# Kernel optimization log

Measured on AMD Instinct MI355X. Metric: run time of the kernel, lower is better.

## Reference

```python
import jax, jax.numpy as jnp
import numpy as np

B, M = 1024, 200000
D_IN, DIM, D_OUT = 256, 128, 10
T = 1.0
EPS = 1e-7


def setup_inputs() -> dict:
    key = jax.random.key(0)
    k1, k2, k3, k4, k5 = jax.random.split(key, 5)
    x = jax.random.normal(k1, (B, D_IN), dtype=jnp.float32)
    y = jax.random.randint(k2, (B,), 0, D_OUT)
    candidate_x = jax.random.normal(k3, (M, D_IN), dtype=jnp.float32)
    candidate_y = jax.random.randint(k4, (M,), 0, D_OUT)
    W_enc = jax.random.normal(k5, (DIM, D_IN), dtype=jnp.float32) * (1.0 / np.sqrt(D_IN))
    b_enc = jnp.zeros((DIM,), dtype=jnp.float32)
    return {"x": x, "y": y, "candidate_x": candidate_x, "candidate_y": candidate_y,
            "W_enc": W_enc, "b_enc": b_enc, "is_train": 0}


def reference(x, y, candidate_x, candidate_y, W_enc, b_enc, is_train):
    # eval path (is_train == 0): no candidate subsampling, no diagonal masking
    h = x @ W_enc.T + b_enc            # [B, DIM]
    hc = candidate_x @ W_enc.T + b_enc  # [M, DIM]
    # pairwise L2 distance (cdist, p=2)
    sq = jnp.sum(h * h, axis=-1, keepdims=True) + jnp.sum(hc * hc, axis=-1)[None, :] \
         - 2.0 * (h @ hc.T)            # [B, M]
    dist = jnp.sqrt(jnp.maximum(sq, 0.0)) / T
    p = jax.nn.softmax(-dist, axis=-1)  # [B, M]
    y1h = jax.nn.one_hot(candidate_y, D_OUT, dtype=h.dtype)  # [M, D_OUT]
    logits = p @ y1h                    # [B, D_OUT]
    return jnp.log(logits + EPS)
```

## Files before the change

kernel.cpp:

```cpp
#include <hip/hip_runtime.h>
#include <hip/hip_bf16.h>
#include <math.h>

#define B_N   1024
#define M_N   200000
#define DIN   256
#define DIMN  128
#define DOUT  10
#define EPS_F 1e-7f
#define M_PAD 200064
#define NBY   1563
#define CTILES 8
#define NGRP  ((NBY + CTILES - 1)/CTILES)
#define YPAD  200

typedef __bf16 bf16_t;
typedef __bf16 bf16x8 __attribute__((ext_vector_type(8)));
typedef float  f32x4  __attribute__((ext_vector_type(4)));


__global__ void cvt_w_kernel(const float* __restrict__ W, bf16_t* __restrict__ Wb){
    int i = blockIdx.x*256 + threadIdx.x;
    if (i < DIMN*DIN) Wb[i] = (bf16_t)W[i];
}

__global__ void hist_kernel(const int* __restrict__ cy, int* __restrict__ hist){
    __shared__ int h[DOUT];
    if (threadIdx.x < DOUT) h[threadIdx.x] = 0;
    __syncthreads();
    for (int i = blockIdx.x*blockDim.x + threadIdx.x; i < M_N; i += gridDim.x*blockDim.x)
        atomicAdd(&h[cy[i]], 1);
    __syncthreads();
    if (threadIdx.x < DOUT) atomicAdd(&hist[threadIdx.x*16], h[threadIdx.x]);
}

__global__ void prefix_kernel(const int* __restrict__ hist, int* __restrict__ cs){
    if (threadIdx.x == 0 && blockIdx.x == 0){
        int acc = 0;
        for (int c = 0; c < DOUT; ++c){ cs[c] = acc; acc += hist[c*16]; }
        cs[DOUT] = acc;
    }
}


__global__ __launch_bounds__(256) void encode_kernel(
    const float* __restrict__ src, const bf16_t* __restrict__ Wb,
    bf16_t* __restrict__ out, float* __restrict__ onorm, int N,
    const int* __restrict__ ycls, int* __restrict__ counters,
    const int* __restrict__ cs)
{
    __shared__ bf16_t As[128][136];
    __shared__ int   posL[128];
    __shared__ float nbuf[128][2];
    __shared__ int   cntL[DOUT], baseL[DOUT];
    const int tid = threadIdx.x;
    const int r0  = blockIdx.x*128;

    int myc = -1, myrank = 0;
    if (ycls != nullptr){
        if (tid < DOUT) cntL[tid] = 0;
        __syncthreads();
        if (tid < 128 && r0 + tid < N){
            myc = ycls[r0 + tid];
            myrank = atomicAdd(&cntL[myc], 1);
        }
        __syncthreads();
        if (tid < DOUT && cntL[tid] > 0)
            baseL[tid] = atomicAdd(&counters[tid*16], cntL[tid]);
        __syncthreads();
    }
    if (tid < 128)
        posL[tid] = (myc >= 0) ? (cs[myc] + baseL[myc] + myrank) : (r0 + tid);

    const int lane = tid & 63, wid = tid >> 6;
    const int wr = wid >> 1, wc = wid & 1;
    const int l15 = lane & 15, quad = lane >> 4;
    const int cbase = wc*64;

    bf16x8 ball[2][4];
    #pragma unroll
    for (int kh = 0; kh < 2; ++kh)
        #pragma unroll
        for (int ks = 0; ks < 4; ++ks){
            ball[kh][ks] = *(const bf16x8*)(Wb + (size_t)(cbase + 0*16 + l15)*DIN + kh*128 + ks*32 + quad*8);
        }

    f32x4 acc[4][4] = {};
    #pragma unroll
    for (int kh = 0; kh < 2; ++kh){
        __syncthreads();
        #pragma unroll
        for (int i = 0; i < 8; ++i){
            int idx = i*256 + tid;
            int row = idx >> 4;
            int col = (idx & 15)*8;
            int rr  = r0 + row; if (rr > N-1) rr = N-1;
            const float4* p4 = (const float4*)(src + (size_t)rr*DIN + kh*128 + col);
            float4 f0 = p4[0], f1 = p4[1];
            bf16x8 v;
            v[0]=(bf16_t)f0.x; v[1]=(bf16_t)f0.y; v[2]=(bf16_t)f0.z; v[3]=(bf16_t)f0.w;
            v[4]=(bf16_t)f1.x; v[5]=(bf16_t)f1.y; v[6]=(bf16_t)f1.z; v[7]=(bf16_t)f1.w;
            *(bf16x8*)&As[row][col] = v;
        }
        __syncthreads();
        #pragma unroll
        for (int ks = 0; ks < 4; ++ks){
            const int k  = ks*32 + quad*8;
            const int kg = kh*128 + k;
            bf16x8 a[4], b[4];
            b[0] = ball[kh][ks];
            #pragma unroll
            for (int ct = 1; ct < 4; ++ct)
                b[ct] = *(const bf16x8*)(Wb + (size_t)(cbase + ct*16 + l15)*DIN + kg);
            #pragma unroll
            for (int rt = 0; rt < 4; ++rt)
                a[rt] = *(const bf16x8*)&As[wr*64 + rt*16 + l15][k];
            #pragma unroll
            for (int rt = 0; rt < 4; ++rt)
                #pragma unroll
                for (int ct = 0; ct < 4; ++ct)
                    acc[rt][ct] = __builtin_amdgcn_mfma_f32_16x16x32_bf16(a[rt], b[ct], acc[rt][ct], 0, 0, 0);
        }
    }

    float np[4][4];
    #pragma unroll
    for (int rt = 0; rt < 4; ++rt)
        #pragma unroll
        for (int r = 0; r < 4; ++r){
            float s = 0.f;
            #pragma unroll
            for (int ct = 0; ct < 4; ++ct){ float v = acc[rt][ct][r]; s += v*v; }
            np[rt][r] = s;
        }
    #pragma unroll
    for (int m = 1; m < 16; m <<= 1)
        #pragma unroll
        for (int rt = 0; rt < 4; ++rt)
            #pragma unroll
            for (int r = 0; r < 4; ++r)
                np[rt][r] += __shfl_xor(np[rt][r], m, 64);
    if (l15 == 0){
        #pragma unroll
        for (int rt = 0; rt < 4; ++rt)
            #pragma unroll
            for (int r = 0; r < 4; ++r)
                nbuf[wr*64 + rt*16 + quad*4 + r][wc] = np[rt][r];
    }

    __syncthreads();

    #pragma unroll
    for (int rt = 0; rt < 4; ++rt)
        #pragma unroll
        for (int r = 0; r < 4; ++r){
            int rl = wr*64 + rt*16 + quad*4 + r;
            #pragma unroll
            for (int ct = 0; ct < 4; ++ct)
                As[rl][cbase + ct*16 + l15] = (bf16_t)acc[rt][ct][r];
        }
    __syncthreads();

    {
        const int rsub = tid >> 4;
        const int cpos = (tid & 15)*8;
        #pragma unroll
        for (int p = 0; p < 8; ++p){
            int rl = p*16 + rsub;
            size_t rowp = (size_t)posL[rl]*DIMN;
            *(bf16x8*)(out + rowp + cpos) = *(const bf16x8*)&As[rl][cpos];
        }
    }
    if (tid < 128){
        int rs = r0 + tid;
        if (rs < N) onorm[posL[tid]] = nbuf[tid][0] + nbuf[tid][1];
    }
}


__device__ __forceinline__ void gld_lds16(const bf16_t* g, bf16_t* l){
    __builtin_amdgcn_global_load_lds((const __attribute__((address_space(1))) void*)g,
                                     (__attribute__((address_space(3))) void*)l, 16, 0, 0);
}

__device__ __forceinline__ void bfly16(float (&s)[2][4]){
    #pragma unroll
    for (int m = 1; m < 16; m <<= 1)
        #pragma unroll
        for (int rt = 0; rt < 2; ++rt)
            #pragma unroll
            for (int r = 0; r < 4; ++r)
                s[rt][r] += __shfl_xor(s[rt][r], m, 64);
}

__device__ __forceinline__ void flushC(float (&s)[2][4], int c, int rbase,
                                       int quad, int l15, float* __restrict__ accG){
    bfly16(s);
    if (l15 == 0){
        #pragma unroll
        for (int rt = 0; rt < 2; ++rt)
            #pragma unroll
            for (int r = 0; r < 4; ++r)
                atomicAdd(&accG[(size_t)(rbase + rt*16 + quad*4 + r)*16 + c], s[rt][r]);
    }
}

__global__ __launch_bounds__(512, 4) void fused_kernel(
    const bf16_t* __restrict__ hb, const bf16_t* __restrict__ hcb,
    const float* __restrict__ hn, const float* __restrict__ hcn,
    const int* __restrict__ csg, float* __restrict__ accG)
{
    const int lin = blockIdx.y*8 + blockIdx.x;
    const int i8  = lin & 7;
    const int t   = lin >> 3;
    const int q   = t >> 3;
    const int r8  = t & 7;
    const int bx  = r8;
    const int yg  = q*8 + i8;
    if (yg >= NGRP) return;

    __shared__ bf16_t Bs0[128][128];
    __shared__ bf16_t Bs1[128][128];
    const int tid = threadIdx.x;
    const int lane = tid & 63, wid = tid >> 6;
    const int wr = wid >> 1, wc = wid & 1;
    const int l15 = lane & 15, quad = lane >> 4;
    const int rbase = bx*128 + wr*32;

    bf16x8 a[4][2];
    #pragma unroll
    for (int ks = 0; ks < 4; ++ks)
        #pragma unroll
        for (int rt = 0; rt < 2; ++rt)
            a[ks][rt] = *(const bf16x8*)(hb + (size_t)(rbase + rt*16 + l15)*DIMN + ks*32 + quad*8);

    float hnv[2][4];
    #pragma unroll
    for (int rt = 0; rt < 2; ++rt)
        #pragma unroll
        for (int r = 0; r < 4; ++r)
            hnv[rt][r] = hn[rbase + rt*16 + quad*4 + r];

    int cseg[DOUT+1];
    #pragma unroll
    for (int i = 0; i <= DOUT; ++i) cseg[i] = __builtin_amdgcn_readfirstlane(csg[i]);

    const int by0 = yg*CTILES;
    int nt = NBY - by0; if (nt > CTILES) nt = CTILES;

    float s[2][4] = {};
    int curC = -1;

    auto stage = [&](bf16_t (&Bsb)[128][128], int by){
        const int cb = by*128;
        #pragma unroll
        for (int i = 0; i < 4; ++i){
            int c   = i*512 + tid;
            int col = c >> 4, j = c & 15;
            int cc  = cb + col; if (cc > M_N-1) cc = M_N-1;
            const bf16_t* g = hcb + (size_t)cc*DIMN + ((j ^ (col & 7)) << 3);
            bf16_t* l = &Bsb[0][0] + ((i*512 + (wid << 6)) << 3);
            gld_lds16(g, l);
        }
    };

    auto compute = [&](const bf16_t (&Bsb)[128][128], int by){
        const int cbase0 = by*128;
        f32x4 acc[2][4] = {};
        const char* bsb = (const char*)&Bsb[0][0];
        #pragma unroll
        for (int ks = 0; ks < 4; ++ks){
            bf16x8 b[4];
            #pragma unroll
            for (int ct = 0; ct < 4; ++ct){
                int row = wc*64 + ct*16 + l15;
                int off = (row << 8) + ((((ks << 6) + (quad << 4))) ^ ((l15 & 7) << 4));
                b[ct] = *(const bf16x8*)(bsb + off);
            }
            #pragma unroll
            for (int rt = 0; rt < 2; ++rt)
                #pragma unroll
                for (int ct = 0; ct < 4; ++ct)
                    acc[rt][ct] = __builtin_amdgcn_mfma_f32_16x16x32_bf16(a[ks][rt], b[ct], acc[rt][ct], 0, 0, 0);
        }

        float hcnv[4];
        #pragma unroll
        for (int ct = 0; ct < 4; ++ct){
            int cc = cbase0 + wc*64 + ct*16 + l15;
            hcnv[ct] = (cc < M_N) ? hcn[cc] : 1e30f;
        }
        #pragma unroll
        for (int rt = 0; rt < 2; ++rt)
            #pragma unroll
            for (int ct = 0; ct < 4; ++ct)
                #pragma unroll
                for (int r = 0; r < 4; ++r){
                    float sq = fmaxf(fmaf(-2.0f, acc[rt][ct][r], hnv[rt][r] + hcnv[ct]), 0.0f);
                    acc[rt][ct][r] = __expf(-__builtin_amdgcn_sqrtf(sq));
                }

        const int lastc = min(cbase0 + 127, M_N - 1);
        int cLo = 0, cHi = 0;
        #pragma unroll
        for (int c = 1; c < DOUT; ++c){
            if (cbase0 >= cseg[c]) cLo = c;
            if (lastc  >= cseg[c]) cHi = c;
        }

        if (cLo == curC && cHi == curC){
            #pragma unroll
            for (int rt = 0; rt < 2; ++rt)
                #pragma unroll
                for (int r = 0; r < 4; ++r){
                    float v0 = acc[rt][0][r] + acc[rt][1][r];
                    float v1 = acc[rt][2][r] + acc[rt][3][r];
                    s[rt][r] += v0 + v1;
                }
        } else {
            if (curC >= 0) flushC(s, curC, rbase, quad, l15, accG);
            #pragma unroll
            for (int rt = 0; rt < 2; ++rt)
                #pragma unroll
                for (int r = 0; r < 4; ++r) s[rt][r] = 0.f;
            for (int c = cLo; c <= cHi; ++c){
                const int s0 = cseg[c], s1 = cseg[c+1];
                float m[2][4];
                #pragma unroll
                for (int rt = 0; rt < 2; ++rt)
                    #pragma unroll
                    for (int r = 0; r < 4; ++r){
                        float v = 0.f;
                        #pragma unroll
                        for (int ct = 0; ct < 4; ++ct){
                            int cc = cbase0 + wc*64 + ct*16 + l15;
                            v += (cc >= s0 && cc < s1) ? acc[rt][ct][r] : 0.f;
                        }
                        m[rt][r] = v;
                    }
                if (c == cHi){
                    #pragma unroll
                    for (int rt = 0; rt < 2; ++rt)
                        #pragma unroll
                        for (int r = 0; r < 4; ++r) s[rt][r] = m[rt][r];
                    curC = cHi;
                } else {
                    flushC(m, c, rbase, quad, l15, accG);
                }
            }
        }
    };

    stage(Bs0, by0);
    __syncthreads();

    #pragma unroll 1
    for (int tp = 0; tp < CTILES/2; ++tp){
        int t0 = tp*2;
        if (t0 >= nt) break;
        if (t0 + 1 < nt) stage(Bs1, by0 + t0 + 1);
        compute(Bs0, by0 + t0);
        __syncthreads();
        int t1 = t0 + 1;
        if (t1 >= nt) break;
        if (t1 + 1 < nt) stage(Bs0, by0 + t1 + 1);
        compute(Bs1, by0 + t1);
        __syncthreads();
    }
    if (curC >= 0) flushC(s, curC, rbase, quad, l15, accG);
}

__global__ void finalize_kernel(const float* __restrict__ accG, float* __restrict__ out){
    int b = blockIdx.x*blockDim.x + threadIdx.x;
    if (b < B_N){
        float v[DOUT]; float den = 0.f;
        #pragma unroll
        for (int c = 0; c < DOUT; ++c){ v[c] = accG[b*16 + c]; den += v[c]; }
        float inv = (den > 0.f) ? 1.0f/den : 0.f;
        #pragma unroll
        for (int c = 0; c < DOUT; ++c) out[b*DOUT + c] = logf(v[c]*inv + EPS_F);
    }
}


extern "C" void kernel_launch(void* const* d_in, const int* in_sizes, int n_in,
                              void* d_out, int out_size, void* d_ws, size_t ws_size,
                              hipStream_t stream)
{
    const float* x  = (const float*)d_in[0];
    const float* cx = (const float*)d_in[2];
    const int*   cy = (const int*)d_in[3];
    const float* W  = (const float*)d_in[4];
    float* out = (float*)d_out;

    char* w = (char*)d_ws;
    size_t off = 0;
    bf16_t* hcb = (bf16_t*)(w + off); off += (size_t)M_PAD*DIMN*2;
    bf16_t* hb  = (bf16_t*)(w + off); off += (size_t)B_N*DIMN*2;
    float*  hcn = (float*) (w + off); off += (size_t)M_PAD*4;
    float*  hn  = (float*) (w + off); off += (size_t)B_N*4;
    bf16_t* Wb  = (bf16_t*)(w + off); off += (size_t)DIMN*DIN*2;
    size_t zoff = off;
    float* accG = (float*)(w + off); off += (size_t)B_N*16*4;
    int* hist     = (int*)(w + off); off += 16*DOUT*4;
    int* counters = (int*)(w + off); off += 16*DOUT*4;
    int* csg      = (int*)(w + off); off += 64;
    size_t zsize = off - zoff;

    hipMemsetAsync(w + zoff, 0, zsize, stream);
    cvt_w_kernel<<<dim3((DIMN*DIN + 255)/256), dim3(256), 0, stream>>>(W, Wb);
    hist_kernel<<<dim3(256), dim3(256), 0, stream>>>(cy, hist);
    prefix_kernel<<<dim3(1), dim3(1), 0, stream>>>(hist, csg);
    encode_kernel<<<dim3(M_PAD/128), dim3(256), 0, stream>>>(cx, Wb, hcb, hcn, M_N, cy, counters, csg);
    encode_kernel<<<dim3(B_N/128), dim3(256), 0, stream>>>(x, Wb, hb, hn, B_N, nullptr, nullptr, nullptr);
    fused_kernel<<<dim3(8, YPAD), dim3(512), 0, stream>>>(hb, hcb, hn, hcn, csg, accG);
    finalize_kernel<<<dim3((B_N + 255)/256), dim3(256), 0, stream>>>(accG, out);
}
```

Before: 482.4 us.

## Software-pipeline MFMA and epilogue across tiles, fold exp2 scaling, merge encode launches

```diff
diff --git a/kernel.cpp b/kernel.cpp
--- a/kernel.cpp
+++ b/kernel.cpp
@@ -9,14 +9,26 @@
 #define DOUT  10
 #define EPS_F 1e-7f
 #define M_PAD 200064
+#define MBLK  1563
 #define NBY   1563
 #define CTILES 8
 #define NGRP  ((NBY + CTILES - 1)/CTILES)
 #define YPAD  200
+#define L2E2  2.0813689810056077f
 
 typedef __bf16 bf16_t;
 typedef __bf16 bf16x8 __attribute__((ext_vector_type(8)));
 typedef float  f32x4  __attribute__((ext_vector_type(4)));
+
+__device__ __forceinline__ float fast_exp2(float x){
+#if __has_builtin(__builtin_amdgcn_exp2f)
+    return __builtin_amdgcn_exp2f(x);
+#else
+    float r;
+    asm("v_exp_f32 %0, %1" : "=v"(r) : "v"(x));
+    return r;
+#endif
+}
 
 
 __global__ void cvt_w_kernel(const float* __restrict__ W, bf16_t* __restrict__ Wb){
@@ -44,9 +56,11 @@
 
 
 __global__ __launch_bounds__(256) void encode_kernel(
-    const float* __restrict__ src, const bf16_t* __restrict__ Wb,
-    bf16_t* __restrict__ out, float* __restrict__ onorm, int N,
-    const int* __restrict__ ycls, int* __restrict__ counters,
+    const float* __restrict__ cx, const float* __restrict__ xb,
+    const bf16_t* __restrict__ Wb,
+    bf16_t* __restrict__ hcb, float* __restrict__ hcn,
+    bf16_t* __restrict__ hb,  float* __restrict__ hn,
+    const int* __restrict__ cy, int* __restrict__ counters,
     const int* __restrict__ cs)
 {
     __shared__ bf16_t As[128][136];
@@ -54,7 +68,13 @@
     __shared__ float nbuf[128][2];
     __shared__ int   cntL[DOUT], baseL[DOUT];
     const int tid = threadIdx.x;
-    const int r0  = blockIdx.x*128;
+
+    const float* src; bf16_t* out; float* onorm; int N; const int* ycls; int r0;
+    if ((int)blockIdx.x < MBLK){
+        src = cx; out = hcb; onorm = hcn; N = M_N; ycls = cy; r0 = blockIdx.x*128;
+    } else {
+        src = xb; out = hb;  onorm = hn;  N = B_N; ycls = nullptr; r0 = (blockIdx.x - MBLK)*128;
+    }
 
     int myc = -1, myrank = 0;
     if (ycls != nullptr){
@@ -81,9 +101,8 @@
     #pragma unroll
     for (int kh = 0; kh < 2; ++kh)
         #pragma unroll
-        for (int ks = 0; ks < 4; ++ks){
-            ball[kh][ks] = *(const bf16x8*)(Wb + (size_t)(cbase + 0*16 + l15)*DIN + kh*128 + ks*32 + quad*8);
-        }
+        for (int ks = 0; ks < 4; ++ks)
+            ball[kh][ks] = *(const bf16x8*)(Wb + (size_t)(cbase + l15)*DIN + kh*128 + ks*32 + quad*8);
 
     f32x4 acc[4][4] = {};
     #pragma unroll
@@ -173,7 +192,7 @@
     }
     if (tid < 128){
         int rs = r0 + tid;
-        if (rs < N) onorm[posL[tid]] = nbuf[tid][0] + nbuf[tid][1];
+        if (rs < N) onorm[posL[tid]] = (nbuf[tid][0] + nbuf[tid][1]) * L2E2;
     }
 }
 
@@ -251,23 +270,28 @@
     float s[2][4] = {};
     int curC = -1;
 
-    auto stage = [&](bf16_t (&Bsb)[128][128], int by){
-        const int cb = by*128;
+    auto stage = [&](bf16_t* Bsb, int by){
+        const bf16_t* base = hcb + (size_t)by*128*DIMN;
         #pragma unroll
         for (int i = 0; i < 4; ++i){
-            int c   = i*512 + tid;
+            int c = i*512 + tid;
             int col = c >> 4, j = c & 15;
-            int cc  = cb + col; if (cc > M_N-1) cc = M_N-1;
-            const bf16_t* g = hcb + (size_t)cc*DIMN + ((j ^ (col & 7)) << 3);
-            bf16_t* l = &Bsb[0][0] + ((i*512 + (wid << 6)) << 3);
-            gld_lds16(g, l);
+            const bf16_t* g = base + (size_t)col*DIMN + ((j ^ (col & 7)) << 3);
+            gld_lds16(g, Bsb + ((i*512 + (wid << 6)) << 3));
         }
     };
 
-    auto compute = [&](const bf16_t (&Bsb)[128][128], int by){
+    auto loadhc = [&](float (&hcv)[4], int by){
         const int cbase0 = by*128;
-        f32x4 acc[2][4] = {};
-        const char* bsb = (const char*)&Bsb[0][0];
+        #pragma unroll
+        for (int ct = 0; ct < 4; ++ct){
+            int cc = cbase0 + wc*64 + ct*16 + l15;
+            hcv[ct] = (cc < M_N) ? hcn[cc] : 1e30f;
+        }
+    };
+
+    auto mfma_tile = [&](const bf16_t* Bsb, f32x4 (&acc)[2][4]){
+        const char* bsb = (const char*)Bsb;
         #pragma unroll
         for (int ks = 0; ks < 4; ++ks){
             bf16x8 b[4];
@@ -283,21 +307,18 @@
                 for (int ct = 0; ct < 4; ++ct)
                     acc[rt][ct] = __builtin_amdgcn_mfma_f32_16x16x32_bf16(a[ks][rt], b[ct], acc[rt][ct], 0, 0, 0);
         }
-
-        float hcnv[4];
-        #pragma unroll
-        for (int ct = 0; ct < 4; ++ct){
-            int cc = cbase0 + wc*64 + ct*16 + l15;
-            hcnv[ct] = (cc < M_N) ? hcn[cc] : 1e30f;
-        }
+    };
+
+    auto epi = [&](f32x4 (&acc)[2][4], int by, const float (&hcv)[4]){
+        const int cbase0 = by*128;
         #pragma unroll
         for (int rt = 0; rt < 2; ++rt)
             #pragma unroll
             for (int ct = 0; ct < 4; ++ct)
                 #pragma unroll
                 for (int r = 0; r < 4; ++r){
-                    float sq = fmaxf(fmaf(-2.0f, acc[rt][ct][r], hnv[rt][r] + hcnv[ct]), 0.0f);
-                    acc[rt][ct][r] = __expf(-__builtin_amdgcn_sqrtf(sq));
+                    float sq = fmaxf(fmaf(-2.0f*L2E2, acc[rt][ct][r], hnv[rt][r] + hcv[ct]), 0.0f);
+                    acc[rt][ct][r] = fast_exp2(-__builtin_amdgcn_sqrtf(sq));
                 }
 
         const int lastc = min(cbase0 + 127, M_N - 1);
@@ -351,21 +372,54 @@
         }
     };
 
-    stage(Bs0, by0);
+    f32x4 accA[2][4], accB[2][4];
+    float hcA[4], hcB[4];
+
+    stage(&Bs0[0][0], by0);
+    __syncthreads();
+
+    if (1 < nt) stage(&Bs1[0][0], by0 + 1);
+    loadhc(hcA, by0);
+    #pragma unroll
+    for (int rt = 0; rt < 2; ++rt)
+        #pragma unroll
+        for (int ct = 0; ct < 4; ++ct) accA[rt][ct] = (f32x4){0.f,0.f,0.f,0.f};
+    mfma_tile(&Bs0[0][0], accA);
     __syncthreads();
 
     #pragma unroll 1
-    for (int tp = 0; tp < CTILES/2; ++tp){
-        int t0 = tp*2;
-        if (t0 >= nt) break;
-        if (t0 + 1 < nt) stage(Bs1, by0 + t0 + 1);
-        compute(Bs0, by0 + t0);
-        __syncthreads();
-        int t1 = t0 + 1;
-        if (t1 >= nt) break;
-        if (t1 + 1 < nt) stage(Bs0, by0 + t1 + 1);
-        compute(Bs1, by0 + t1);
-        __syncthreads();
+    for (int tt = 1; tt + 1 < nt; tt += 2){
+        if (tt + 1 < nt) stage(&Bs0[0][0], by0 + tt + 1);
+        loadhc(hcB, by0 + tt);
+        #pragma unroll
+        for (int rt = 0; rt < 2; ++rt)
+            #pragma unroll
+            for (int ct = 0; ct < 4; ++ct) accB[rt][ct] = (f32x4){0.f,0.f,0.f,0.f};
+        mfma_tile(&Bs1[0][0], accB);
+        epi(accA, by0 + tt - 1, hcA);
+        __syncthreads();
+        if (tt + 2 < nt) stage(&Bs1[0][0], by0 + tt + 2);
+        loadhc(hcA, by0 + tt + 1);
+        #pragma unroll
+        for (int rt = 0; rt < 2; ++rt)
+            #pragma unroll
+            for (int ct = 0; ct < 4; ++ct) accA[rt][ct] = (f32x4){0.f,0.f,0.f,0.f};
+        mfma_tile(&Bs0[0][0], accA);
+        epi(accB, by0 + tt, hcB);
+        __syncthreads();
+    }
+
+    if (!(nt & 1)){
+        loadhc(hcB, by0 + nt - 1);
+        #pragma unroll
+        for (int rt = 0; rt < 2; ++rt)
+            #pragma unroll
+            for (int ct = 0; ct < 4; ++ct) accB[rt][ct] = (f32x4){0.f,0.f,0.f,0.f};
+        mfma_tile(&Bs1[0][0], accB);
+        epi(accA, by0 + nt - 2, hcA);
+        epi(accB, by0 + nt - 1, hcB);
+    } else {
+        epi(accA, by0 + nt - 1, hcA);
     }
     if (curC >= 0) flushC(s, curC, rbase, quad, l15, accG);
 }
@@ -411,8 +465,8 @@
     cvt_w_kernel<<<dim3((DIMN*DIN + 255)/256), dim3(256), 0, stream>>>(W, Wb);
     hist_kernel<<<dim3(256), dim3(256), 0, stream>>>(cy, hist);
     prefix_kernel<<<dim3(1), dim3(1), 0, stream>>>(hist, csg);
-    encode_kernel<<<dim3(M_PAD/128), dim3(256), 0, stream>>>(cx, Wb, hcb, hcn, M_N, cy, counters, csg);
-    encode_kernel<<<dim3(B_N/128), dim3(256), 0, stream>>>(x, Wb, hb, hn, B_N, nullptr, nullptr, nullptr);
+    encode_kernel<<<dim3(MBLK + B_N/128), dim3(256), 0, stream>>>(
+        cx, x, Wb, hcb, hcn, hb, hn, cy, counters, csg);
     fused_kernel<<<dim3(8, YPAD), dim3(512), 0, stream>>>(hb, hcb, hn, hcn, csg, accG);
     finalize_kernel<<<dim3((B_N + 255)/256), dim3(256), 0, stream>>>(accG, out);
 }
```

Measured after the change: 623.8 us. +29.3%, slower.
